# Kernel tuning notes

Measured on AMD Instinct MI355X. Metric: run time of the kernel, lower is better.

Reference implementation:

```python
import jax, jax.numpy as jnp
import numpy as np

MEX_C = 2.0 / (np.sqrt(3.0) * np.pi ** 0.25)

def mexican_hat(z):
    return MEX_C * (z * z - 1.0) * jnp.exp(-0.5 * z * z)

def setup_inputs() -> dict:
    key = jax.random.key(0)
    ks = jax.random.split(key, 5)
    B, T, D, O = 4, 2048, 128, 128
    x = jax.random.normal(ks[0], (B, T, D), dtype=jnp.float32)
    # init like torch: scale ~ U(0.5,1.5), translation ~ U(-0.5,0.5), kaiming-ish weights
    scale = jax.random.uniform(ks[1], (O, D), dtype=jnp.float32, minval=0.5, maxval=1.5)
    translation = jax.random.uniform(ks[2], (O, D), dtype=jnp.float32, minval=-0.5, maxval=0.5)
    bound = 1.0 / np.sqrt(D)
    wavelet_weights = jax.random.uniform(ks[3], (O, D), dtype=jnp.float32, minval=-bound, maxval=bound)
    base_w = jax.random.uniform(ks[4], (O, D), dtype=jnp.float32, minval=-bound, maxval=bound)
    ln_gamma = jnp.ones((D,), dtype=jnp.float32)
    ln_beta = jnp.zeros((D,), dtype=jnp.float32)
    return {"x": x, "scale": scale, "translation": translation,
            "wavelet_weights": wavelet_weights, "base_w": base_w,
            "ln_gamma": ln_gamma, "ln_beta": ln_beta}

def reference(x, scale, translation, wavelet_weights, base_w, ln_gamma, ln_beta):
    B, T, D = x.shape
    O = wavelet_weights.shape[0]
    # LayerNorm over last dim (eps = 1e-5, torch default)
    mu = jnp.mean(x, axis=-1, keepdims=True)
    var = jnp.mean((x - mu) ** 2, axis=-1, keepdims=True)
    x_norm = (x - mu) / jnp.sqrt(var + 1e-5) * ln_gamma + ln_beta
    x_flat = x_norm.reshape(B * T, D)                      # (N, D)
    s = jax.nn.softplus(scale) + 0.1                       # (O, D)
    # broadcast intermediate (N, O, D) — the memory-bound path
    z = (x_flat[:, None, :] - translation[None]) / s[None]
    w = jnp.clip(mexican_hat(z), -10.0, 10.0)              # (N, O, D)
    wavelet_out = jnp.einsum('nod,od->no', w, wavelet_weights)
    base_out = x.reshape(B * T, D) @ base_w.T              # base uses raw x
    out = wavelet_out + jax.nn.silu(base_out)
    return out.reshape(B, T, O)
```

## Files before the change

### kernel.cpp

```cpp
#include <hip/hip_runtime.h>


#define D_DIM 128
#define O_DIM 128
#define ROWS  32
#define BLOCK 512
#define XPAD  289

#define C1     0.72134752f
#define SQRT_C 0.84932180f
#define WWK    1.2023651f
#define LOG2E  1.44269504f

typedef float v2f __attribute__((ext_vector_type(2)));

__device__ __forceinline__ void wk_pair(float sc, float tr, float w_w, float b_w,
                                        float& wx, float& wy, float& wz, float& wb) {
    float sp  = fmaxf(sc, 0.0f) + __logf(1.0f + __expf(-fabsf(sc)));
    float is2 = SQRT_C / (sp + 0.1f);
    wx = tr * is2; wy = is2; wz = w_w * WWK; wb = b_w;
}

__global__ __launch_bounds__(256) void wavekan_prep(
    const float* __restrict__ scale,
    const float* __restrict__ trans,
    const float* __restrict__ ww,
    const float* __restrict__ bw,
    float4* __restrict__ wsW)
{
    int idx = blockIdx.x * blockDim.x + threadIdx.x;
    if (idx >= O_DIM * (D_DIM / 2)) return;
    int o = idx >> 6;
    int p = idx & 63;
    int i0 = o * D_DIM + p * 2;
    float wx0, wy0, wz0, wb0, wx1, wy1, wz1, wb1;
    wk_pair(scale[i0],     trans[i0],     ww[i0],     bw[i0],     wx0, wy0, wz0, wb0);
    wk_pair(scale[i0 + 1], trans[i0 + 1], ww[i0 + 1], bw[i0 + 1], wx1, wy1, wz1, wb1);
    wsW[(p * O_DIM + o) * 2 + 0] = make_float4(wx0, wx1, wy0, wy1);
    wsW[(p * O_DIM + o) * 2 + 1] = make_float4(wz0, wz1, wb0, wb1);
}

template<bool USE_WS>
__global__ __launch_bounds__(BLOCK, 2) void wavekan_main(
    const float* __restrict__ x,
    const float* __restrict__ scale,
    const float* __restrict__ trans,
    const float* __restrict__ ww,
    const float* __restrict__ bw,
    const float* __restrict__ gamma,
    const float* __restrict__ beta,
    const float4* __restrict__ wsW,
    float* __restrict__ out,
    int N)
{
    __shared__ float4 s_ln4[4 * XPAD];
    __shared__ float4 s_rw4[4 * XPAD];

    const int tid  = threadIdx.x;
    const int lane = tid & 63;
    const int wv   = tid >> 6;
    const int o    = wv * 16 + (lane & 15);
    const int dg   = lane >> 4;
    const int row0 = blockIdx.x * ROWS;

    float4 wA[16], wB[16];
    if (USE_WS) {
        #pragma unroll
        for (int k = 0; k < 16; ++k) {
            const int p = dg * 16 + k;
            wA[k] = wsW[(p * O_DIM + o) * 2 + 0];
            wB[k] = wsW[(p * O_DIM + o) * 2 + 1];
        }
    } else {
        #pragma unroll
        for (int k = 0; k < 16; ++k) {
            const int i0 = o * D_DIM + dg * 32 + 2 * k;
            float wx0, wy0, wz0, wb0, wx1, wy1, wz1, wb1;
            wk_pair(scale[i0],     trans[i0],     ww[i0],     bw[i0],     wx0, wy0, wz0, wb0);
            wk_pair(scale[i0 + 1], trans[i0 + 1], ww[i0 + 1], bw[i0 + 1], wx1, wy1, wz1, wb1);
            wA[k] = make_float4(wx0, wx1, wy0, wy1);
            wB[k] = make_float4(wz0, wz1, wb0, wb1);
        }
    }

    {
        const int r    = tid >> 4;
        const int j    = tid & 15;
        const int d0   = j * 8;
        const int grow = row0 + r;

        float4 va = make_float4(0.f, 0.f, 0.f, 0.f);
        float4 vb = make_float4(0.f, 0.f, 0.f, 0.f);
        if (grow < N) {
            va = *reinterpret_cast<const float4*>(x + (size_t)grow * D_DIM + d0);
            vb = *reinterpret_cast<const float4*>(x + (size_t)grow * D_DIM + d0 + 4);
        }
        float sum = ((va.x + va.y) + (va.z + va.w)) + ((vb.x + vb.y) + (vb.z + vb.w));
        float ssq = ((va.x * va.x + va.y * va.y) + (va.z * va.z + va.w * va.w))
                  + ((vb.x * vb.x + vb.y * vb.y) + (vb.z * vb.z + vb.w * vb.w));
        #pragma unroll
        for (int m = 1; m < 16; m <<= 1) {
            sum += __shfl_xor(sum, m, 64);
            ssq += __shfl_xor(ssq, m, 64);
        }
        const float mean = sum * (1.0f / D_DIM);
        const float var  = ssq * (1.0f / D_DIM) - mean * mean;
        const float rstd = rsqrtf(var + 1e-5f);

        float4 ga = *reinterpret_cast<const float4*>(gamma + d0);
        float4 gb = *reinterpret_cast<const float4*>(gamma + d0 + 4);
        float4 ba = *reinterpret_cast<const float4*>(beta + d0);
        float4 bb = *reinterpret_cast<const float4*>(beta + d0 + 4);

        const int wdg = j >> 2;
        const int q0  = (j & 3) * 2;
        const int ib  = wdg * XPAD + r * 9 + q0;

        s_ln4[ib]     = make_float4((va.x - mean) * rstd * ga.x + ba.x,
                                    (va.y - mean) * rstd * ga.y + ba.y,
                                    (va.z - mean) * rstd * ga.z + ba.z,
                                    (va.w - mean) * rstd * ga.w + ba.w);
        s_ln4[ib + 1] = make_float4((vb.x - mean) * rstd * gb.x + bb.x,
                                    (vb.y - mean) * rstd * gb.y + bb.y,
                                    (vb.z - mean) * rstd * gb.z + bb.z,
                                    (vb.w - mean) * rstd * gb.w + bb.w);
        s_rw4[ib]     = va;
        s_rw4[ib + 1] = vb;
    }
    __syncthreads();

    #pragma unroll 1
    for (int r = 0; r < ROWS; ++r) {
        const int xb = dg * XPAD + r * 9;
        v2f aw = {0.f, 0.f};
        v2f ab = {0.f, 0.f};
        #pragma unroll
        for (int k4 = 0; k4 < 8; ++k4) {
            float4 xl = s_ln4[xb + k4];
            float4 xr = s_rw4[xb + k4];
            float4 a0 = wA[2 * k4],     b0 = wB[2 * k4];
            float4 a1 = wA[2 * k4 + 1], b1 = wB[2 * k4 + 1];

            v2f u, qq, e;
            u  = (v2f){xl.x, xl.y} * (v2f){a0.z, a0.w} - (v2f){a0.x, a0.y};
            qq = u * u;
            e  = (v2f){__builtin_amdgcn_exp2f(-qq.x), __builtin_amdgcn_exp2f(-qq.y)};
            aw += ((qq - C1) * e) * (v2f){b0.x, b0.y};
            ab += (v2f){xr.x, xr.y} * (v2f){b0.z, b0.w};

            u  = (v2f){xl.z, xl.w} * (v2f){a1.z, a1.w} - (v2f){a1.x, a1.y};
            qq = u * u;
            e  = (v2f){__builtin_amdgcn_exp2f(-qq.x), __builtin_amdgcn_exp2f(-qq.y)};
            aw += ((qq - C1) * e) * (v2f){b1.x, b1.y};
            ab += (v2f){xr.z, xr.w} * (v2f){b1.z, b1.w};
        }
        float wav = aw.x + aw.y;
        float bas = ab.x + ab.y;
        wav += __shfl_xor(wav, 16, 64);
        wav += __shfl_xor(wav, 32, 64);
        bas += __shfl_xor(bas, 16, 64);
        bas += __shfl_xor(bas, 32, 64);

        if ((lane < 16) && (row0 + r < N)) {
            float sig = 1.0f / (1.0f + __builtin_amdgcn_exp2f(-LOG2E * bas));
            out[(size_t)(row0 + r) * O_DIM + o] = wav + bas * sig;
        }
    }
}

extern "C" void kernel_launch(void* const* d_in, const int* in_sizes, int n_in,
                              void* d_out, int out_size, void* d_ws, size_t ws_size,
                              hipStream_t stream) {
    const float* x     = (const float*)d_in[0];
    const float* scale = (const float*)d_in[1];
    const float* trans = (const float*)d_in[2];
    const float* ww    = (const float*)d_in[3];
    const float* bw    = (const float*)d_in[4];
    const float* gamma = (const float*)d_in[5];
    const float* beta  = (const float*)d_in[6];
    float* out = (float*)d_out;

    const int N = in_sizes[0] / D_DIM;
    const int grid = (N + ROWS - 1) / ROWS;

    const size_t ws_needed = (size_t)O_DIM * (D_DIM / 2) * 2 * sizeof(float4);
    if (ws_size >= ws_needed) {
        wavekan_prep<<<(O_DIM * (D_DIM / 2) + 255) / 256, 256, 0, stream>>>(
            scale, trans, ww, bw, (float4*)d_ws);
        wavekan_main<true><<<grid, BLOCK, 0, stream>>>(
            x, scale, trans, ww, bw, gamma, beta, (const float4*)d_ws, out, N);
    } else {
        wavekan_main<false><<<grid, BLOCK, 0, stream>>>(
            x, scale, trans, ww, bw, gamma, beta, nullptr, out, N);
    }
}
```

Baseline: 101.1 us.

## Recover base matmul from normalized x and double block size with halved weight registers

Stops staging raw x in shared memory. The base linear term is now rebuilt from the LayerNorm output by algebra: base weights are divided by gamma, and per-row mean and std plus per-output beta/gamma correction sums are applied afterwards. The block grows to 1024 threads with 8 outputs per wave and 8 d-groups, which halves the per-thread weight registers and targets higher occupancy. The costs are an extra shuffle stage per row, and a risk of inaccuracy or division by zero if gamma is near zero.

```diff
diff --git a/kernel.cpp b/kernel.cpp
--- a/kernel.cpp
+++ b/kernel.cpp
@@ -4,8 +4,8 @@
 #define D_DIM 128
 #define O_DIM 128
 #define ROWS  32
-#define BLOCK 512
-#define XPAD  289
+#define BLOCK 1024
+#define XSTR  161
 
 #define C1     0.72134752f
 #define SQRT_C 0.84932180f
@@ -14,11 +14,13 @@
 
 typedef float v2f __attribute__((ext_vector_type(2)));
 
-__device__ __forceinline__ void wk_pair(float sc, float tr, float w_w, float b_w,
+#define PIN4(v) asm volatile("" : "+v"((v).x), "+v"((v).y), "+v"((v).z), "+v"((v).w))
+
+__device__ __forceinline__ void wk_pair(float sc, float tr, float w_w, float b_wp,
                                         float& wx, float& wy, float& wz, float& wb) {
     float sp  = fmaxf(sc, 0.0f) + __logf(1.0f + __expf(-fabsf(sc)));
     float is2 = SQRT_C / (sp + 0.1f);
-    wx = tr * is2; wy = is2; wz = w_w * WWK; wb = b_w;
+    wx = tr * is2; wy = is2; wz = w_w * WWK; wb = b_wp;
 }
 
 __global__ __launch_bounds__(256) void wavekan_prep(
@@ -26,22 +28,24 @@
     const float* __restrict__ trans,
     const float* __restrict__ ww,
     const float* __restrict__ bw,
+    const float* __restrict__ gamma,
     float4* __restrict__ wsW)
 {
     int idx = blockIdx.x * blockDim.x + threadIdx.x;
     if (idx >= O_DIM * (D_DIM / 2)) return;
     int o = idx >> 6;
     int p = idx & 63;
-    int i0 = o * D_DIM + p * 2;
+    int d0 = 2 * p;
+    int i0 = o * D_DIM + d0;
     float wx0, wy0, wz0, wb0, wx1, wy1, wz1, wb1;
-    wk_pair(scale[i0],     trans[i0],     ww[i0],     bw[i0],     wx0, wy0, wz0, wb0);
-    wk_pair(scale[i0 + 1], trans[i0 + 1], ww[i0 + 1], bw[i0 + 1], wx1, wy1, wz1, wb1);
+    wk_pair(scale[i0],     trans[i0],     ww[i0],     bw[i0]     / gamma[d0],     wx0, wy0, wz0, wb0);
+    wk_pair(scale[i0 + 1], trans[i0 + 1], ww[i0 + 1], bw[i0 + 1] / gamma[d0 + 1], wx1, wy1, wz1, wb1);
     wsW[(p * O_DIM + o) * 2 + 0] = make_float4(wx0, wx1, wy0, wy1);
     wsW[(p * O_DIM + o) * 2 + 1] = make_float4(wz0, wz1, wb0, wb1);
 }
 
 template<bool USE_WS>
-__global__ __launch_bounds__(BLOCK, 2) void wavekan_main(
+__global__ __launch_bounds__(BLOCK, 4) void wavekan_main(
     const float* __restrict__ x,
     const float* __restrict__ scale,
     const float* __restrict__ trans,
@@ -53,53 +57,51 @@
     float* __restrict__ out,
     int N)
 {
-    __shared__ float4 s_ln4[4 * XPAD];
-    __shared__ float4 s_rw4[4 * XPAD];
+    __shared__ float4 s_ln4[8 * XSTR];
+    __shared__ float2 s_stat[ROWS];
 
     const int tid  = threadIdx.x;
     const int lane = tid & 63;
     const int wv   = tid >> 6;
-    const int o    = wv * 16 + (lane & 15);
-    const int dg   = lane >> 4;
+    const int o    = wv * 8 + (lane & 7);
+    const int dg   = lane >> 3;
     const int row0 = blockIdx.x * ROWS;
 
-    float4 wA[16], wB[16];
+    float4 wA[8], wB[8];
     if (USE_WS) {
         #pragma unroll
-        for (int k = 0; k < 16; ++k) {
-            const int p = dg * 16 + k;
+        for (int k = 0; k < 8; ++k) {
+            const int p = dg * 8 + k;
             wA[k] = wsW[(p * O_DIM + o) * 2 + 0];
             wB[k] = wsW[(p * O_DIM + o) * 2 + 1];
         }
     } else {
         #pragma unroll
-        for (int k = 0; k < 16; ++k) {
-            const int i0 = o * D_DIM + dg * 32 + 2 * k;
+        for (int k = 0; k < 8; ++k) {
+            const int d0 = dg * 16 + 2 * k;
+            const int i0 = o * D_DIM + d0;
             float wx0, wy0, wz0, wb0, wx1, wy1, wz1, wb1;
-            wk_pair(scale[i0],     trans[i0],     ww[i0],     bw[i0],     wx0, wy0, wz0, wb0);
-            wk_pair(scale[i0 + 1], trans[i0 + 1], ww[i0 + 1], bw[i0 + 1], wx1, wy1, wz1, wb1);
+            wk_pair(scale[i0],     trans[i0],     ww[i0],     bw[i0]     / gamma[d0],     wx0, wy0, wz0, wb0);
+            wk_pair(scale[i0 + 1], trans[i0 + 1], ww[i0 + 1], bw[i0 + 1] / gamma[d0 + 1], wx1, wy1, wz1, wb1);
             wA[k] = make_float4(wx0, wx1, wy0, wy1);
             wB[k] = make_float4(wz0, wz1, wb0, wb1);
         }
     }
 
     {
-        const int r    = tid >> 4;
-        const int j    = tid & 15;
-        const int d0   = j * 8;
+        const int r    = tid >> 5;
+        const int j    = tid & 31;
+        const int d0j  = j * 4;
         const int grow = row0 + r;
 
-        float4 va = make_float4(0.f, 0.f, 0.f, 0.f);
-        float4 vb = make_float4(0.f, 0.f, 0.f, 0.f);
-        if (grow < N) {
-            va = *reinterpret_cast<const float4*>(x + (size_t)grow * D_DIM + d0);
-            vb = *reinterpret_cast<const float4*>(x + (size_t)grow * D_DIM + d0 + 4);
-        }
-        float sum = ((va.x + va.y) + (va.z + va.w)) + ((vb.x + vb.y) + (vb.z + vb.w));
-        float ssq = ((va.x * va.x + va.y * va.y) + (va.z * va.z + va.w * va.w))
-                  + ((vb.x * vb.x + vb.y * vb.y) + (vb.z * vb.z + vb.w * vb.w));
-        #pragma unroll
-        for (int m = 1; m < 16; m <<= 1) {
+        float4 v4 = make_float4(0.f, 0.f, 0.f, 0.f);
+        if (grow < N)
+            v4 = *reinterpret_cast<const float4*>(x + (size_t)grow * D_DIM + d0j);
+
+        float sum = (v4.x + v4.y) + (v4.z + v4.w);
+        float ssq = (v4.x * v4.x + v4.y * v4.y) + (v4.z * v4.z + v4.w * v4.w);
+        #pragma unroll
+        for (int m = 1; m < 32; m <<= 1) {
             sum += __shfl_xor(sum, m, 64);
             ssq += __shfl_xor(ssq, m, 64);
         }
@@ -107,63 +109,74 @@
         const float var  = ssq * (1.0f / D_DIM) - mean * mean;
         const float rstd = rsqrtf(var + 1e-5f);
 
-        float4 ga = *reinterpret_cast<const float4*>(gamma + d0);
-        float4 gb = *reinterpret_cast<const float4*>(gamma + d0 + 4);
-        float4 ba = *reinterpret_cast<const float4*>(beta + d0);
-        float4 bb = *reinterpret_cast<const float4*>(beta + d0 + 4);
-
-        const int wdg = j >> 2;
-        const int q0  = (j & 3) * 2;
-        const int ib  = wdg * XPAD + r * 9 + q0;
-
-        s_ln4[ib]     = make_float4((va.x - mean) * rstd * ga.x + ba.x,
-                                    (va.y - mean) * rstd * ga.y + ba.y,
-                                    (va.z - mean) * rstd * ga.z + ba.z,
-                                    (va.w - mean) * rstd * ga.w + ba.w);
-        s_ln4[ib + 1] = make_float4((vb.x - mean) * rstd * gb.x + bb.x,
-                                    (vb.y - mean) * rstd * gb.y + bb.y,
-                                    (vb.z - mean) * rstd * gb.z + bb.z,
-                                    (vb.w - mean) * rstd * gb.w + bb.w);
-        s_rw4[ib]     = va;
-        s_rw4[ib + 1] = vb;
-    }
+        float4 g4 = *reinterpret_cast<const float4*>(gamma + d0j);
+        float4 b4 = *reinterpret_cast<const float4*>(beta + d0j);
+
+        s_ln4[(j >> 2) * XSTR + r * 5 + (j & 3)] =
+            make_float4((v4.x - mean) * rstd * g4.x + b4.x,
+                        (v4.y - mean) * rstd * g4.y + b4.y,
+                        (v4.z - mean) * rstd * g4.z + b4.z,
+                        (v4.w - mean) * rstd * g4.w + b4.w);
+        if (j == 0)
+            s_stat[r] = make_float2(mean, sqrtf(var + 1e-5f));
+    }
+
+    float cb = 0.f, sb = 0.f;
+    #pragma unroll
+    for (int k = 0; k < 8; ++k) {
+        float2 bt = *reinterpret_cast<const float2*>(beta  + dg * 16 + 2 * k);
+        float2 gt = *reinterpret_cast<const float2*>(gamma + dg * 16 + 2 * k);
+        cb += bt.x * wB[k].z + bt.y * wB[k].w;
+        sb += gt.x * wB[k].z + gt.y * wB[k].w;
+    }
+    cb += __shfl_xor(cb, 8, 64); cb += __shfl_xor(cb, 16, 64); cb += __shfl_xor(cb, 32, 64);
+    sb += __shfl_xor(sb, 8, 64); sb += __shfl_xor(sb, 16, 64); sb += __shfl_xor(sb, 32, 64);
+
+    #pragma unroll
+    for (int k = 0; k < 8; ++k) {
+        PIN4(wA[k]);
+        PIN4(wB[k]);
+    }
+
     __syncthreads();
 
     #pragma unroll 1
     for (int r = 0; r < ROWS; ++r) {
-        const int xb = dg * XPAD + r * 9;
+        const int xb = dg * XSTR + r * 5;
         v2f aw = {0.f, 0.f};
         v2f ab = {0.f, 0.f};
         #pragma unroll
-        for (int k4 = 0; k4 < 8; ++k4) {
+        for (int k4 = 0; k4 < 4; ++k4) {
             float4 xl = s_ln4[xb + k4];
-            float4 xr = s_rw4[xb + k4];
-            float4 a0 = wA[2 * k4],     b0 = wB[2 * k4];
-            float4 a1 = wA[2 * k4 + 1], b1 = wB[2 * k4 + 1];
+            float4 a0 = wA[2 * k4],     c0 = wB[2 * k4];
+            float4 a1 = wA[2 * k4 + 1], c1 = wB[2 * k4 + 1];
 
             v2f u, qq, e;
             u  = (v2f){xl.x, xl.y} * (v2f){a0.z, a0.w} - (v2f){a0.x, a0.y};
             qq = u * u;
             e  = (v2f){__builtin_amdgcn_exp2f(-qq.x), __builtin_amdgcn_exp2f(-qq.y)};
-            aw += ((qq - C1) * e) * (v2f){b0.x, b0.y};
-            ab += (v2f){xr.x, xr.y} * (v2f){b0.z, b0.w};
+            aw += ((qq - C1) * e) * (v2f){c0.x, c0.y};
+            ab += (v2f){xl.x, xl.y} * (v2f){c0.z, c0.w};
 
             u  = (v2f){xl.z, xl.w} * (v2f){a1.z, a1.w} - (v2f){a1.x, a1.y};
             qq = u * u;
             e  = (v2f){__builtin_amdgcn_exp2f(-qq.x), __builtin_amdgcn_exp2f(-qq.y)};
-            aw += ((qq - C1) * e) * (v2f){b1.x, b1.y};
-            ab += (v2f){xr.z, xr.w} * (v2f){b1.z, b1.w};
+            aw += ((qq - C1) * e) * (v2f){c1.x, c1.y};
+            ab += (v2f){xl.z, xl.w} * (v2f){c1.z, c1.w};
         }
         float wav = aw.x + aw.y;
-        float bas = ab.x + ab.y;
-        wav += __shfl_xor(wav, 16, 64);
-        wav += __shfl_xor(wav, 32, 64);
-        bas += __shfl_xor(bas, 16, 64);
-        bas += __shfl_xor(bas, 32, 64);
-
-        if ((lane < 16) && (row0 + r < N)) {
-            float sig = 1.0f / (1.0f + __builtin_amdgcn_exp2f(-LOG2E * bas));
-            out[(size_t)(row0 + r) * O_DIM + o] = wav + bas * sig;
+        float A   = ab.x + ab.y;
+        wav += __shfl_xor(wav, 8, 64); wav += __shfl_xor(wav, 16, 64); wav += __shfl_xor(wav, 32, 64);
+        A   += __shfl_xor(A,   8, 64); A   += __shfl_xor(A,   16, 64); A   += __shfl_xor(A,   32, 64);
+
+        if (dg == 0) {
+            const int grow = row0 + r;
+            if (grow < N) {
+                float2 st   = s_stat[r];
+                float  base = (A - cb) * st.y + st.x * sb;
+                float  sig  = 1.0f / (1.0f + __builtin_amdgcn_exp2f(-LOG2E * base));
+                out[(size_t)grow * O_DIM + o] = wav + base * sig;
+            }
         }
     }
 }
@@ -186,7 +199,7 @@
     const size_t ws_needed = (size_t)O_DIM * (D_DIM / 2) * 2 * sizeof(float4);
     if (ws_size >= ws_needed) {
         wavekan_prep<<<(O_DIM * (D_DIM / 2) + 255) / 256, 256, 0, stream>>>(
-            scale, trans, ww, bw, (float4*)d_ws);
+            scale, trans, ww, bw, gamma, (float4*)d_ws);
         wavekan_main<true><<<grid, BLOCK, 0, stream>>>(
             x, scale, trans, ww, bw, gamma, beta, (const float4*)d_ws, out, N);
     } else {
```

Result: no change. 102.4 us (+1.2%).
